# Kernel tuning notes

Measured on AMD Instinct MI355X. Metric: run time of the kernel, lower is better.

Reference implementation:

```python
import jax, jax.numpy as jnp
import numpy as np

NUM_VERTEX = 1448
C = 256


def _decode(latent, eye_labels, left_mu, left_delta, right_mu, right_delta):
    # latent: [B, C, H, W] -> global average pool -> [B, C]
    lat = jnp.mean(latent, axis=(-2, -1))
    # batched decode against both eye models, select per-sample by eye label
    left = lat @ left_delta.T + left_mu[:, 0]    # [B, 3*N]
    right = lat @ right_delta.T + right_mu[:, 0]  # [B, 3*N]
    pts = jnp.where(eye_labels[:, None] == 1, right, left)
    return pts.reshape(lat.shape[0], NUM_VERTEX, 3)  # [B, N, 3]


def _cdist(a, b):
    # Euclidean distance via the norm trick; a,b: [B, N, 3]
    a2 = jnp.sum(a * a, axis=-1)  # [B, N]
    b2 = jnp.sum(b * b, axis=-1)  # [B, M]
    d2 = a2[:, :, None] + b2[:, None, :] - 2.0 * jnp.einsum('bnd,bmd->bnm', a, b)
    return jnp.sqrt(jnp.maximum(d2, 1e-12))


def setup_inputs() -> dict:
    key = jax.random.key(0)
    ks = jax.random.split(key, 8)
    B, H, W = 64, 8, 8
    inputs = jax.random.normal(ks[0], (B, C, H, W), dtype=jnp.float32)
    targets = jax.random.normal(ks[1], (B, C, H, W), dtype=jnp.float32)
    eye_labels = jax.random.randint(ks[2], (B,), 0, 2)
    left_mu = jax.random.normal(ks[3], (3 * NUM_VERTEX, 1), dtype=jnp.float32)
    left_delta = jax.random.normal(ks[4], (3 * NUM_VERTEX, C), dtype=jnp.float32) * 0.1
    right_mu = jax.random.normal(ks[5], (3 * NUM_VERTEX, 1), dtype=jnp.float32)
    right_delta = jax.random.normal(ks[6], (3 * NUM_VERTEX, C), dtype=jnp.float32) * 0.1
    return {"inputs": inputs, "targets": targets, "eye_labels": eye_labels,
            "left_mu": left_mu, "left_delta": left_delta,
            "right_mu": right_mu, "right_delta": right_delta}


def reference(inputs, targets, eye_labels, left_mu, left_delta, right_mu, right_delta):
    pts_in = _decode(inputs, eye_labels, left_mu, left_delta, right_mu, right_delta)
    pts_tg = _decode(targets, eye_labels, left_mu, left_delta, right_mu, right_delta)
    d = _cdist(pts_in, pts_tg)  # [B, N, N]
    dist_1 = jnp.mean(jnp.min(d, axis=-1))
    dist_2 = jnp.mean(jnp.min(d, axis=-2))
    return dist_1 + dist_2
```

## Files before the change

kernel.cpp:

```cpp
#include <hip/hip_runtime.h>

#define NV 1448
#define JD 4344
#define CC 256
#define BB 64
#define QQ 128
#define QCOLS 362
#define NROW (2 * BB * NV)

__global__ __launch_bounds__(256) void pool_kernel(const float* __restrict__ inp,
                                                   const float* __restrict__ tgt,
                                                   float* __restrict__ latT,
                                                   unsigned long long* __restrict__ acc) {
    int gid  = blockIdx.x * 256 + threadIdx.x;
    if (gid == 0) { acc[0] = 0ull; acc[1] = 0ull; }
    int lane = gid & 15;
    int row  = gid >> 4;
    if (row >= 2 * BB * CC) return;
    int t  = row >> 14;
    int bc = row & 16383;
    const float* src = (t ? tgt : inp) + (size_t)bc * 64;
    float4 v = reinterpret_cast<const float4*>(src)[lane];
    float s = (v.x + v.y) + (v.z + v.w);
    s += __shfl_xor(s, 1);
    s += __shfl_xor(s, 2);
    s += __shfl_xor(s, 4);
    s += __shfl_xor(s, 8);
    if (lane == 0) {
        int b = bc >> 8, c = bc & 255;
        latT[c * QQ + t * BB + b] = s * (1.0f / 64.0f);
    }
}

__global__ __launch_bounds__(64, 4) void decode_kernel(const float* __restrict__ latT,
                                                       const float* __restrict__ muL,
                                                       const float* __restrict__ deltaL,
                                                       const float* __restrict__ muR,
                                                       const float* __restrict__ deltaR,
                                                       const int* __restrict__ labels,
                                                       float* __restrict__ pts3) {
    const int jt = blockIdx.x;
    const int L  = blockIdx.y;
    const int qh = blockIdx.z;
    const float* __restrict__ delta = L ? deltaR : deltaL;
    const float* __restrict__ mu    = L ? muR : muL;
    const int j0   = jt * 16;
    const int lane = threadIdx.x;
    const int jl   = lane & 3;
    const int qg   = lane >> 2;

    __shared__ float AsT[32][16];
    __shared__ float Bs[32][64];

    float acc[4][4];
#pragma unroll
    for (int u = 0; u < 4; ++u)
#pragma unroll
        for (int v = 0; v < 4; ++v) acc[u][v] = 0.f;

    const float4* latT4 = reinterpret_cast<const float4*>(latT);

    for (int kc = 0; kc < CC; kc += 32) {
        __syncthreads();
#pragma unroll
        for (int it = 0; it < 2; ++it) {
            int idx = it * 64 + lane;
            int kq  = idx & 7;
            int r   = idx >> 3;
            int j   = j0 + r;
            float4 v = make_float4(0.f, 0.f, 0.f, 0.f);
            if (j < JD)
                v = *reinterpret_cast<const float4*>(delta + (size_t)j * CC + kc + kq * 4);
            AsT[kq * 4 + 0][r] = v.x;
            AsT[kq * 4 + 1][r] = v.y;
            AsT[kq * 4 + 2][r] = v.z;
            AsT[kq * 4 + 3][r] = v.w;
        }
#pragma unroll
        for (int it = 0; it < 8; ++it) {
            int idx = it * 64 + lane;
            int qi  = idx & 15;
            int k   = idx >> 4;
            reinterpret_cast<float4*>(&Bs[k][0])[qi] =
                latT4[(size_t)(kc + k) * 32 + qh * 16 + qi];
        }
        __syncthreads();

#pragma unroll
        for (int k4 = 0; k4 < 32; k4 += 4) {
#pragma unroll
            for (int kk = 0; kk < 4; ++kk) {
                float4 a = *reinterpret_cast<const float4*>(&AsT[k4 + kk][jl * 4]);
                float4 b = *reinterpret_cast<const float4*>(&Bs[k4 + kk][qg * 4]);
                float av[4] = {a.x, a.y, a.z, a.w};
                float bv[4] = {b.x, b.y, b.z, b.w};
#pragma unroll
                for (int u = 0; u < 4; ++u)
#pragma unroll
                    for (int v = 0; v < 4; ++v)
                        acc[u][v] = fmaf(av[u], bv[v], acc[u][v]);
            }
        }
    }

    int j = j0 + jl * 4;
    if (j + 3 < JD) {
        float4 m = *reinterpret_cast<const float4*>(mu + j);
#pragma unroll
        for (int v = 0; v < 4; ++v) {
            int q = qh * 64 + qg * 4 + v;
            int b = q & 63;
            if (labels[b] == L) {
                float4 o = make_float4(acc[0][v] + m.x, acc[1][v] + m.y,
                                       acc[2][v] + m.z, acc[3][v] + m.w);
                *reinterpret_cast<float4*>(pts3 + (size_t)q * JD + j) = o;
            }
        }
    }
}

__global__ __launch_bounds__(256) void chamfer_kernel(const float* __restrict__ pts3,
                                                      float* __restrict__ pmin) {
    const int chunk = blockIdx.x;
    const int b     = blockIdx.y;
    const int dir   = blockIdx.z >> 2;
    const int q     = blockIdx.z & 3;
    const int qa = dir * BB + b;
    const int qb = (1 - dir) * BB + b;
    const float* __restrict__ A3 = pts3 + (size_t)qa * JD;
    const float* __restrict__ B3 = pts3 + (size_t)qb * JD + q * (QCOLS * 3);

    __shared__ float4 Bs[QCOLS];
    const int tid = threadIdx.x;
    for (int i = tid; i < QCOLS; i += 256) {
        float x = B3[3 * i], y = B3[3 * i + 1], z = B3[3 * i + 2];
        Bs[i] = make_float4(-2.f * x, -2.f * y, -2.f * z, fmaf(x, x, fmaf(y, y, z * z)));
    }
    __syncthreads();

    int r0 = chunk * 512 + tid;
    int r1 = r0 + 256;
    float a0x = 0.f, a0y = 0.f, a0z = 0.f, a0w = 0.f;
    float a1x = 0.f, a1y = 0.f, a1z = 0.f, a1w = 0.f;
    if (r0 < NV) {
        a0x = A3[3 * r0]; a0y = A3[3 * r0 + 1]; a0z = A3[3 * r0 + 2];
        a0w = fmaf(a0x, a0x, fmaf(a0y, a0y, a0z * a0z));
    }
    if (r1 < NV) {
        a1x = A3[3 * r1]; a1y = A3[3 * r1 + 1]; a1z = A3[3 * r1 + 2];
        a1w = fmaf(a1x, a1x, fmaf(a1y, a1y, a1z * a1z));
    }
    float m0 = 1e30f, m1 = 1e30f;

#pragma unroll 2
    for (int m = 0; m < QCOLS; m += 2) {
        float4 b0 = Bs[m];
        float4 b1 = Bs[m + 1];
        float d00 = fmaf(b0.x, a0x, fmaf(b0.y, a0y, fmaf(b0.z, a0z, b0.w)));
        float d01 = fmaf(b1.x, a0x, fmaf(b1.y, a0y, fmaf(b1.z, a0z, b1.w)));
        asm("v_min3_f32 %0, %0, %1, %2" : "+v"(m0) : "v"(d00), "v"(d01));
        float d10 = fmaf(b0.x, a1x, fmaf(b0.y, a1y, fmaf(b0.z, a1z, b0.w)));
        float d11 = fmaf(b1.x, a1x, fmaf(b1.y, a1y, fmaf(b1.z, a1z, b1.w)));
        asm("v_min3_f32 %0, %0, %1, %2" : "+v"(m1) : "v"(d10), "v"(d11));
    }

    size_t base = (size_t)q * NROW + (size_t)qa * NV;
    if (r0 < NV) pmin[base + r0] = m0 + a0w;
    if (r1 < NV) pmin[base + r1] = m1 + a1w;
}

__global__ __launch_bounds__(256) void combine_kernel(const float* __restrict__ pmin,
                                                      unsigned long long* __restrict__ acc,
                                                      float* __restrict__ out) {
    const int base = blockIdx.x * 724;
    const int tid  = threadIdx.x;
    float s = 0.f;
#pragma unroll
    for (int it = 0; it < 3; ++it) {
        int idx = it * 256 + tid;
        if (idx < 724) {
            int g = base + idx;
            float v = fminf(fminf(pmin[g], pmin[g + NROW]),
                            fminf(pmin[g + 2 * NROW], pmin[g + 3 * NROW]));
            s += sqrtf(fmaxf(v, 1e-12f));
        }
    }
    s += __shfl_xor(s, 1);
    s += __shfl_xor(s, 2);
    s += __shfl_xor(s, 4);
    s += __shfl_xor(s, 8);
    s += __shfl_xor(s, 16);
    s += __shfl_xor(s, 32);
    __shared__ float wsum[4];
    if ((tid & 63) == 0) wsum[tid >> 6] = s;
    __syncthreads();
    if (tid == 0) {
        float bs = wsum[0] + wsum[1] + wsum[2] + wsum[3];
        unsigned long long qv = (unsigned long long)((double)bs * 16777216.0);
        atomicAdd(acc, qv);
        __threadfence();
        unsigned long long done = atomicAdd(acc + 1, 1ull);
        if (done == 255) {
            __threadfence();
            unsigned long long total = atomicAdd(acc, 0ull);
            out[0] = (float)((double)total * (0x1p-24 / (64.0 * 1448.0)));
        }
    }
}

extern "C" void kernel_launch(void* const* d_in, const int* in_sizes, int n_in,
                              void* d_out, int out_size, void* d_ws, size_t ws_size,
                              hipStream_t stream) {
    const float* inp    = (const float*)d_in[0];
    const float* tgt    = (const float*)d_in[1];
    const int*   labels = (const int*)d_in[2];
    const float* muL    = (const float*)d_in[3];
    const float* deltaL = (const float*)d_in[4];
    const float* muR    = (const float*)d_in[5];
    const float* deltaR = (const float*)d_in[6];
    float* out = (float*)d_out;

    char* ws = (char*)d_ws;
    float* latT = (float*)ws;
    float* pts3 = (float*)(ws + 131072);
    float* pmin = (float*)(ws + 131072 + 2224128);
    unsigned long long* acc = (unsigned long long*)(ws + 131072 + 2224128 + 2965504);

    hipLaunchKernelGGL(pool_kernel, dim3(2048), dim3(256), 0, stream, inp, tgt, latT, acc);
    hipLaunchKernelGGL(decode_kernel, dim3(272, 2, 2), dim3(64), 0, stream,
                       latT, muL, deltaL, muR, deltaR, labels, pts3);
    hipLaunchKernelGGL(chamfer_kernel, dim3(3, 64, 8), dim3(256), 0, stream,
                       pts3, pmin);
    hipLaunchKernelGGL(combine_kernel, dim3(256), dim3(256), 0, stream, pmin, acc, out);
}
```

Baseline: 63.06 us.

## Split decode K reduction across four waves with LDS cross-wave reduction

```diff
diff --git a/kernel.cpp b/kernel.cpp
--- a/kernel.cpp
+++ b/kernel.cpp
@@ -32,25 +32,28 @@
     }
 }
 
-__global__ __launch_bounds__(64, 4) void decode_kernel(const float* __restrict__ latT,
-                                                       const float* __restrict__ muL,
-                                                       const float* __restrict__ deltaL,
-                                                       const float* __restrict__ muR,
-                                                       const float* __restrict__ deltaR,
-                                                       const int* __restrict__ labels,
-                                                       float* __restrict__ pts3) {
+__global__ __launch_bounds__(256, 4) void decode_kernel(const float* __restrict__ latT,
+                                                        const float* __restrict__ muL,
+                                                        const float* __restrict__ deltaL,
+                                                        const float* __restrict__ muR,
+                                                        const float* __restrict__ deltaR,
+                                                        const int* __restrict__ labels,
+                                                        float* __restrict__ pts3) {
     const int jt = blockIdx.x;
     const int L  = blockIdx.y;
     const int qh = blockIdx.z;
     const float* __restrict__ delta = L ? deltaR : deltaL;
     const float* __restrict__ mu    = L ? muR : muL;
     const int j0   = jt * 16;
-    const int lane = threadIdx.x;
+    const int tid  = threadIdx.x;
+    const int w    = tid >> 6;
+    const int lane = tid & 63;
     const int jl   = lane & 3;
     const int qg   = lane >> 2;
 
-    __shared__ float AsT[32][16];
-    __shared__ float Bs[32][64];
+    __shared__ float lds[10240];
+    float* AsT = lds + w * 2560;
+    float* Bs  = AsT + 512;
 
     float acc[4][4];
 #pragma unroll
@@ -60,8 +63,9 @@
 
     const float4* latT4 = reinterpret_cast<const float4*>(latT);
 
-    for (int kc = 0; kc < CC; kc += 32) {
-        __syncthreads();
+#pragma unroll
+    for (int c = 0; c < 2; ++c) {
+        const int kc = w * 32 + c * 128;
 #pragma unroll
         for (int it = 0; it < 2; ++it) {
             int idx = it * 64 + lane;
@@ -71,27 +75,25 @@
             float4 v = make_float4(0.f, 0.f, 0.f, 0.f);
             if (j < JD)
                 v = *reinterpret_cast<const float4*>(delta + (size_t)j * CC + kc + kq * 4);
-            AsT[kq * 4 + 0][r] = v.x;
-            AsT[kq * 4 + 1][r] = v.y;
-            AsT[kq * 4 + 2][r] = v.z;
-            AsT[kq * 4 + 3][r] = v.w;
+            AsT[(kq * 4 + 0) * 16 + r] = v.x;
+            AsT[(kq * 4 + 1) * 16 + r] = v.y;
+            AsT[(kq * 4 + 2) * 16 + r] = v.z;
+            AsT[(kq * 4 + 3) * 16 + r] = v.w;
         }
 #pragma unroll
         for (int it = 0; it < 8; ++it) {
             int idx = it * 64 + lane;
             int qi  = idx & 15;
             int k   = idx >> 4;
-            reinterpret_cast<float4*>(&Bs[k][0])[qi] =
+            reinterpret_cast<float4*>(Bs)[k * 16 + qi] =
                 latT4[(size_t)(kc + k) * 32 + qh * 16 + qi];
         }
-        __syncthreads();
-
 #pragma unroll
         for (int k4 = 0; k4 < 32; k4 += 4) {
 #pragma unroll
             for (int kk = 0; kk < 4; ++kk) {
-                float4 a = *reinterpret_cast<const float4*>(&AsT[k4 + kk][jl * 4]);
-                float4 b = *reinterpret_cast<const float4*>(&Bs[k4 + kk][qg * 4]);
+                float4 a = *reinterpret_cast<const float4*>(&AsT[(k4 + kk) * 16 + jl * 4]);
+                float4 b = *reinterpret_cast<const float4*>(&Bs[(k4 + kk) * 64 + qg * 4]);
                 float av[4] = {a.x, a.y, a.z, a.w};
                 float bv[4] = {b.x, b.y, b.z, b.w};
 #pragma unroll
@@ -103,17 +105,34 @@
         }
     }
 
-    int j = j0 + jl * 4;
-    if (j + 3 < JD) {
-        float4 m = *reinterpret_cast<const float4*>(mu + j);
-#pragma unroll
-        for (int v = 0; v < 4; ++v) {
-            int q = qh * 64 + qg * 4 + v;
-            int b = q & 63;
-            if (labels[b] == L) {
-                float4 o = make_float4(acc[0][v] + m.x, acc[1][v] + m.y,
-                                       acc[2][v] + m.z, acc[3][v] + m.w);
-                *reinterpret_cast<float4*>(pts3 + (size_t)q * JD + j) = o;
+    __syncthreads();
+    float4* red4 = reinterpret_cast<float4*>(lds);
+#pragma unroll
+    for (int u = 0; u < 4; ++u)
+        red4[lane * 17 + w * 4 + u] = make_float4(acc[u][0], acc[u][1], acc[u][2], acc[u][3]);
+    __syncthreads();
+
+    if (w == 0) {
+#pragma unroll
+        for (int u = 0; u < 4; ++u) {
+#pragma unroll
+            for (int ww = 1; ww < 4; ++ww) {
+                float4 p = red4[lane * 17 + ww * 4 + u];
+                acc[u][0] += p.x; acc[u][1] += p.y; acc[u][2] += p.z; acc[u][3] += p.w;
+            }
+        }
+        int j = j0 + jl * 4;
+        if (j + 3 < JD) {
+            float4 m = *reinterpret_cast<const float4*>(mu + j);
+#pragma unroll
+            for (int v = 0; v < 4; ++v) {
+                int q = qh * 64 + qg * 4 + v;
+                int b = q & 63;
+                if (labels[b] == L) {
+                    float4 o = make_float4(acc[0][v] + m.x, acc[1][v] + m.y,
+                                           acc[2][v] + m.z, acc[3][v] + m.w);
+                    *reinterpret_cast<float4*>(pts3 + (size_t)q * JD + j) = o;
+                }
             }
         }
     }
@@ -227,7 +246,7 @@
     unsigned long long* acc = (unsigned long long*)(ws + 131072 + 2224128 + 2965504);
 
     hipLaunchKernelGGL(pool_kernel, dim3(2048), dim3(256), 0, stream, inp, tgt, latT, acc);
-    hipLaunchKernelGGL(decode_kernel, dim3(272, 2, 2), dim3(64), 0, stream,
+    hipLaunchKernelGGL(decode_kernel, dim3(272, 2, 2), dim3(256), 0, stream,
                        latT, muL, deltaL, muR, deltaR, labels, pts3);
     hipLaunchKernelGGL(chamfer_kernel, dim3(3, 64, 8), dim3(256), 0, stream,
                        pts3, pmin);
```

After: 123.9 us. 96.4% more time.

## Compact decode columns by eye label to skip unselected eye-model products

Applied to the files above, without the earlier changes.

```diff
diff --git a/kernel.cpp b/kernel.cpp
--- a/kernel.cpp
+++ b/kernel.cpp
@@ -10,10 +10,25 @@
 
 __global__ __launch_bounds__(256) void pool_kernel(const float* __restrict__ inp,
                                                    const float* __restrict__ tgt,
-                                                   float* __restrict__ latT,
-                                                   unsigned long long* __restrict__ acc) {
+                                                   float* __restrict__ latQ,
+                                                   unsigned long long* __restrict__ acc,
+                                                   const int* __restrict__ labels,
+                                                   int* __restrict__ qperm,
+                                                   int* __restrict__ gside) {
     int gid  = blockIdx.x * 256 + threadIdx.x;
-    if (gid == 0) { acc[0] = 0ull; acc[1] = 0ull; }
+    if (gid == 0) {
+        acc[0] = 0ull; acc[1] = 0ull;
+        int pos = 0;
+        for (int q = 0; q < QQ; ++q) if (labels[q & 63] == 0) qperm[pos++] = q;
+        gside[0] = (pos > 0)  ? 0 : -1;
+        gside[1] = (pos > 64) ? 0 : -1;
+        for (int i = pos; i < 128; ++i) qperm[i] = -1;
+        int pos2 = 128;
+        for (int q = 0; q < QQ; ++q) if (labels[q & 63] == 1) qperm[pos2++] = q;
+        gside[2] = (pos2 > 128) ? 1 : -1;
+        gside[3] = (pos2 > 192) ? 1 : -1;
+        for (int i = pos2; i < 256; ++i) qperm[i] = -1;
+    }
     int lane = gid & 15;
     int row  = gid >> 4;
     if (row >= 2 * BB * CC) return;
@@ -28,22 +43,24 @@
     s += __shfl_xor(s, 8);
     if (lane == 0) {
         int b = bc >> 8, c = bc & 255;
-        latT[c * QQ + t * BB + b] = s * (1.0f / 64.0f);
-    }
-}
-
-__global__ __launch_bounds__(64, 4) void decode_kernel(const float* __restrict__ latT,
+        latQ[(size_t)(t * 64 + b) * CC + c] = s * (1.0f / 64.0f);
+    }
+}
+
+__global__ __launch_bounds__(64, 4) void decode_kernel(const float* __restrict__ latQ,
                                                        const float* __restrict__ muL,
                                                        const float* __restrict__ deltaL,
                                                        const float* __restrict__ muR,
                                                        const float* __restrict__ deltaR,
-                                                       const int* __restrict__ labels,
+                                                       const int* __restrict__ qperm,
+                                                       const int* __restrict__ gside,
                                                        float* __restrict__ pts3) {
+    const int g    = blockIdx.y;
+    const int side = gside[g];
+    if (side < 0) return;
     const int jt = blockIdx.x;
-    const int L  = blockIdx.y;
-    const int qh = blockIdx.z;
-    const float* __restrict__ delta = L ? deltaR : deltaL;
-    const float* __restrict__ mu    = L ? muR : muL;
+    const float* __restrict__ delta = side ? deltaR : deltaL;
+    const float* __restrict__ mu    = side ? muR : muL;
     const int j0   = jt * 16;
     const int lane = threadIdx.x;
     const int jl   = lane & 3;
@@ -51,14 +68,17 @@
 
     __shared__ float AsT[32][16];
     __shared__ float Bs[32][64];
+    __shared__ int   qs_sh[64];
+
+    int qmine = qperm[g * 64 + lane];
+    qs_sh[lane] = qmine;
+    const float* __restrict__ brow = latQ + (size_t)(qmine < 0 ? 0 : qmine) * CC;
 
     float acc[4][4];
 #pragma unroll
     for (int u = 0; u < 4; ++u)
 #pragma unroll
         for (int v = 0; v < 4; ++v) acc[u][v] = 0.f;
-
-    const float4* latT4 = reinterpret_cast<const float4*>(latT);
 
     for (int kc = 0; kc < CC; kc += 32) {
         __syncthreads();
@@ -77,12 +97,12 @@
             AsT[kq * 4 + 3][r] = v.w;
         }
 #pragma unroll
-        for (int it = 0; it < 8; ++it) {
-            int idx = it * 64 + lane;
-            int qi  = idx & 15;
-            int k   = idx >> 4;
-            reinterpret_cast<float4*>(&Bs[k][0])[qi] =
-                latT4[(size_t)(kc + k) * 32 + qh * 16 + qi];
+        for (int i = 0; i < 8; ++i) {
+            float4 v = *reinterpret_cast<const float4*>(brow + kc + i * 4);
+            Bs[i * 4 + 0][lane] = v.x;
+            Bs[i * 4 + 1][lane] = v.y;
+            Bs[i * 4 + 2][lane] = v.z;
+            Bs[i * 4 + 3][lane] = v.w;
         }
         __syncthreads();
 
@@ -108,9 +128,8 @@
         float4 m = *reinterpret_cast<const float4*>(mu + j);
 #pragma unroll
         for (int v = 0; v < 4; ++v) {
-            int q = qh * 64 + qg * 4 + v;
-            int b = q & 63;
-            if (labels[b] == L) {
+            int q = qs_sh[qg * 4 + v];
+            if (q >= 0) {
                 float4 o = make_float4(acc[0][v] + m.x, acc[1][v] + m.y,
                                        acc[2][v] + m.z, acc[3][v] + m.w);
                 *reinterpret_cast<float4*>(pts3 + (size_t)q * JD + j) = o;
@@ -221,14 +240,17 @@
     float* out = (float*)d_out;
 
     char* ws = (char*)d_ws;
-    float* latT = (float*)ws;
+    float* latQ = (float*)ws;
     float* pts3 = (float*)(ws + 131072);
     float* pmin = (float*)(ws + 131072 + 2224128);
     unsigned long long* acc = (unsigned long long*)(ws + 131072 + 2224128 + 2965504);
-
-    hipLaunchKernelGGL(pool_kernel, dim3(2048), dim3(256), 0, stream, inp, tgt, latT, acc);
-    hipLaunchKernelGGL(decode_kernel, dim3(272, 2, 2), dim3(64), 0, stream,
-                       latT, muL, deltaL, muR, deltaR, labels, pts3);
+    int* qperm = (int*)((char*)acc + 256);
+    int* gside = qperm + 256;
+
+    hipLaunchKernelGGL(pool_kernel, dim3(2048), dim3(256), 0, stream,
+                       inp, tgt, latQ, acc, labels, qperm, gside);
+    hipLaunchKernelGGL(decode_kernel, dim3(272, 4), dim3(64), 0, stream,
+                       latQ, muL, deltaL, muR, deltaR, qperm, gside, pts3);
     hipLaunchKernelGGL(chamfer_kernel, dim3(3, 64, 8), dim3(256), 0, stream,
                        pts3, pmin);
     hipLaunchKernelGGL(combine_kernel, dim3(256), dim3(256), 0, stream, pmin, acc, out);
```

New measurement: 72.29 us. 14.6% more time.

## Rewrite decode GEMM with bf16 MFMA and bf16 latent layout

Applied to the files above, without the earlier changes.

```diff
diff --git a/kernel.cpp b/kernel.cpp
--- a/kernel.cpp
+++ b/kernel.cpp
@@ -8,9 +8,17 @@
 #define QCOLS 362
 #define NROW (2 * BB * NV)
 
+typedef __bf16 bf16x8 __attribute__((ext_vector_type(8)));
+typedef float  f32x4  __attribute__((ext_vector_type(4)));
+
+__device__ __forceinline__ unsigned f2bf(float f) {
+    unsigned u = __float_as_uint(f);
+    return (u + 0x7FFFu + ((u >> 16) & 1u)) >> 16;
+}
+
 __global__ __launch_bounds__(256) void pool_kernel(const float* __restrict__ inp,
                                                    const float* __restrict__ tgt,
-                                                   float* __restrict__ latT,
+                                                   unsigned short* __restrict__ latQb,
                                                    unsigned long long* __restrict__ acc) {
     int gid  = blockIdx.x * 256 + threadIdx.x;
     if (gid == 0) { acc[0] = 0ull; acc[1] = 0ull; }
@@ -28,92 +36,79 @@
     s += __shfl_xor(s, 8);
     if (lane == 0) {
         int b = bc >> 8, c = bc & 255;
-        latT[c * QQ + t * BB + b] = s * (1.0f / 64.0f);
-    }
-}
-
-__global__ __launch_bounds__(64, 4) void decode_kernel(const float* __restrict__ latT,
-                                                       const float* __restrict__ muL,
-                                                       const float* __restrict__ deltaL,
-                                                       const float* __restrict__ muR,
-                                                       const float* __restrict__ deltaR,
-                                                       const int* __restrict__ labels,
-                                                       float* __restrict__ pts3) {
-    const int jt = blockIdx.x;
-    const int L  = blockIdx.y;
-    const int qh = blockIdx.z;
-    const float* __restrict__ delta = L ? deltaR : deltaL;
-    const float* __restrict__ mu    = L ? muR : muL;
-    const int j0   = jt * 16;
-    const int lane = threadIdx.x;
-    const int jl   = lane & 3;
-    const int qg   = lane >> 2;
-
-    __shared__ float AsT[32][16];
-    __shared__ float Bs[32][64];
-
-    float acc[4][4];
-#pragma unroll
-    for (int u = 0; u < 4; ++u)
-#pragma unroll
-        for (int v = 0; v < 4; ++v) acc[u][v] = 0.f;
-
-    const float4* latT4 = reinterpret_cast<const float4*>(latT);
-
-    for (int kc = 0; kc < CC; kc += 32) {
-        __syncthreads();
-#pragma unroll
-        for (int it = 0; it < 2; ++it) {
-            int idx = it * 64 + lane;
-            int kq  = idx & 7;
-            int r   = idx >> 3;
-            int j   = j0 + r;
-            float4 v = make_float4(0.f, 0.f, 0.f, 0.f);
-            if (j < JD)
-                v = *reinterpret_cast<const float4*>(delta + (size_t)j * CC + kc + kq * 4);
-            AsT[kq * 4 + 0][r] = v.x;
-            AsT[kq * 4 + 1][r] = v.y;
-            AsT[kq * 4 + 2][r] = v.z;
-            AsT[kq * 4 + 3][r] = v.w;
-        }
-#pragma unroll
-        for (int it = 0; it < 8; ++it) {
-            int idx = it * 64 + lane;
-            int qi  = idx & 15;
-            int k   = idx >> 4;
-            reinterpret_cast<float4*>(&Bs[k][0])[qi] =
-                latT4[(size_t)(kc + k) * 32 + qh * 16 + qi];
-        }
-        __syncthreads();
-
-#pragma unroll
-        for (int k4 = 0; k4 < 32; k4 += 4) {
-#pragma unroll
-            for (int kk = 0; kk < 4; ++kk) {
-                float4 a = *reinterpret_cast<const float4*>(&AsT[k4 + kk][jl * 4]);
-                float4 b = *reinterpret_cast<const float4*>(&Bs[k4 + kk][qg * 4]);
-                float av[4] = {a.x, a.y, a.z, a.w};
-                float bv[4] = {b.x, b.y, b.z, b.w};
-#pragma unroll
-                for (int u = 0; u < 4; ++u)
-#pragma unroll
-                    for (int v = 0; v < 4; ++v)
-                        acc[u][v] = fmaf(av[u], bv[v], acc[u][v]);
-            }
-        }
-    }
-
-    int j = j0 + jl * 4;
-    if (j + 3 < JD) {
-        float4 m = *reinterpret_cast<const float4*>(mu + j);
-#pragma unroll
-        for (int v = 0; v < 4; ++v) {
-            int q = qh * 64 + qg * 4 + v;
-            int b = q & 63;
-            if (labels[b] == L) {
-                float4 o = make_float4(acc[0][v] + m.x, acc[1][v] + m.y,
-                                       acc[2][v] + m.z, acc[3][v] + m.w);
-                *reinterpret_cast<float4*>(pts3 + (size_t)q * JD + j) = o;
+        latQb[(size_t)(t * 64 + b) * CC + c] = (unsigned short)f2bf(s * (1.0f / 64.0f));
+    }
+}
+
+__global__ __launch_bounds__(256) void decode_kernel(const unsigned short* __restrict__ latQb,
+                                                     const float* __restrict__ muL,
+                                                     const float* __restrict__ deltaL,
+                                                     const float* __restrict__ muR,
+                                                     const float* __restrict__ deltaR,
+                                                     const int* __restrict__ labels,
+                                                     float* __restrict__ pts3) {
+    const int jt   = blockIdx.x;
+    const int side = blockIdx.y;
+    const int qq   = blockIdx.z;
+    const float* __restrict__ delta = side ? deltaR : deltaL;
+    const float* __restrict__ mu    = side ? muR : muL;
+    const int jb = jt * 64;
+    const int q0 = qq * 32;
+    const int tid  = threadIdx.x;
+    const int w    = tid >> 6;
+    const int lane = tid & 63;
+
+    __shared__ unsigned short dB[64 * 264];
+    __shared__ unsigned short lB[32 * 264];
+
+#pragma unroll
+    for (int i = 0; i < 16; ++i) {
+        int idx = i * 256 + tid;
+        int row = idx >> 6;
+        int ch  = idx & 63;
+        int j   = jb + row;
+        unsigned u0 = 0, u1 = 0;
+        if (j < JD) {
+            float4 v = *reinterpret_cast<const float4*>(delta + (size_t)j * CC + ch * 4);
+            u0 = f2bf(v.x) | (f2bf(v.y) << 16);
+            u1 = f2bf(v.z) | (f2bf(v.w) << 16);
+        }
+        *reinterpret_cast<uint2*>(&dB[row * 264 + ch * 4]) = make_uint2(u0, u1);
+    }
+#pragma unroll
+    for (int i = 0; i < 4; ++i) {
+        int idx = i * 256 + tid;
+        int row = idx >> 5;
+        int ch  = idx & 31;
+        *reinterpret_cast<uint4*>(&lB[row * 264 + ch * 8]) =
+            *reinterpret_cast<const uint4*>(latQb + (size_t)(q0 + row) * CC + ch * 8);
+    }
+    __syncthreads();
+
+    const int col  = lane & 15;
+    const int kgrp = lane >> 4;
+    bf16x8 bfr[8];
+#pragma unroll
+    for (int ks = 0; ks < 8; ++ks)
+        bfr[ks] = *reinterpret_cast<const bf16x8*>(&dB[(w * 16 + col) * 264 + ks * 32 + kgrp * 8]);
+
+    int j = jb + w * 16 + col;
+    float muv = (j < JD) ? mu[j] : 0.f;
+
+#pragma unroll
+    for (int mt = 0; mt < 2; ++mt) {
+        f32x4 acc = {0.f, 0.f, 0.f, 0.f};
+#pragma unroll
+        for (int ks = 0; ks < 8; ++ks) {
+            bf16x8 a = *reinterpret_cast<const bf16x8*>(&lB[(mt * 16 + col) * 264 + ks * 32 + kgrp * 8]);
+            acc = __builtin_amdgcn_mfma_f32_16x16x32_bf16(a, bfr[ks], acc, 0, 0, 0);
+        }
+        if (j < JD) {
+#pragma unroll
+            for (int r = 0; r < 4; ++r) {
+                int q = q0 + mt * 16 + kgrp * 4 + r;
+                if (labels[q & 63] == side)
+                    pts3[(size_t)q * JD + j] = acc[r] + muv;
             }
         }
     }
@@ -221,14 +216,14 @@
     float* out = (float*)d_out;
 
     char* ws = (char*)d_ws;
-    float* latT = (float*)ws;
-    float* pts3 = (float*)(ws + 131072);
-    float* pmin = (float*)(ws + 131072 + 2224128);
-    unsigned long long* acc = (unsigned long long*)(ws + 131072 + 2224128 + 2965504);
-
-    hipLaunchKernelGGL(pool_kernel, dim3(2048), dim3(256), 0, stream, inp, tgt, latT, acc);
-    hipLaunchKernelGGL(decode_kernel, dim3(272, 2, 2), dim3(64), 0, stream,
-                       latT, muL, deltaL, muR, deltaR, labels, pts3);
+    unsigned short* latQb = (unsigned short*)ws;
+    float* pts3 = (float*)(ws + 65536);
+    float* pmin = (float*)(ws + 65536 + 2224128);
+    unsigned long long* acc = (unsigned long long*)(ws + 65536 + 2224128 + 2965504);
+
+    hipLaunchKernelGGL(pool_kernel, dim3(2048), dim3(256), 0, stream, inp, tgt, latQb, acc);
+    hipLaunchKernelGGL(decode_kernel, dim3(68, 2, 4), dim3(256), 0, stream,
+                       latQb, muL, deltaL, muR, deltaR, labels, pts3);
     hipLaunchKernelGGL(chamfer_kernel, dim3(3, 64, 8), dim3(256), 0, stream,
                        pts3, pmin);
     hipLaunchKernelGGL(combine_kernel, dim3(256), dim3(256), 0, stream, pmin, acc, out);
```

Result: faster. 51.91 us (median of 2 runs) (-17.7%).
